# Performance work log

Hardware: AMD Instinct MI355X
Metric: run time of the kernel (lower is better)

The kernel has to match this reference:

```python
import math
import jax, jax.numpy as jnp
import numpy as np

M, D, NL, H, DFF = 14, 128, 2, 4, 512
BS = 256
DK = D // H


def setup_inputs() -> dict:
    key = jax.random.key(0)
    ks = iter(jax.random.split(key, 40))
    def w(shape, s=0.02):
        return jax.random.normal(next(ks), shape, jnp.float32) * s
    return dict(
        src=jax.random.normal(next(ks), (BS, M), jnp.float32),
        t=5,
        fc_w=w((D, 1, 3), 0.3), fc_b=jnp.zeros((D,), jnp.float32),
        gc_w=w((D, 1, 3), 0.3), gc_b=jnp.zeros((D,), jnp.float32),
        ln_w=jnp.ones((D,), jnp.float32), ln_b=jnp.zeros((D,), jnp.float32),
        qw=w((NL, D, D)), qb=jnp.zeros((NL, D), jnp.float32),
        kw=w((NL, D, D)), kb=jnp.zeros((NL, D), jnp.float32),
        vw=w((NL, D, D)), vb=jnp.zeros((NL, D), jnp.float32),
        ow=w((NL, D, D)), ob=jnp.zeros((NL, D), jnp.float32),
        n1a=jnp.ones((NL, D), jnp.float32), n1b=jnp.zeros((NL, D), jnp.float32),
        n2a=jnp.ones((NL, D), jnp.float32), n2b=jnp.zeros((NL, D), jnp.float32),
        w1=w((NL, DFF, D)), b1=jnp.zeros((NL, DFF), jnp.float32),
        w2=w((NL, D, DFF)), b2=jnp.zeros((NL, D), jnp.float32),
        fna=jnp.ones((D,), jnp.float32), fnb=jnp.zeros((D,), jnp.float32),
        out_w=w((1, D)), out_b=jnp.zeros((1,), jnp.float32),
    )


def _conv1d(x, w):  # x [B,1,m], w [O,1,3], padding=1 (SAME)
    return jax.lax.conv_general_dilated(
        x, w, window_strides=(1,), padding=[(1, 1)],
        dimension_numbers=('NCH', 'OIH', 'NCH'))


def _norm(x, a, b, eps=1e-6):
    # torch: alpha*(x-mean)/(std+eps)+bias, std is UNBIASED (ddof=1)
    mu = x.mean(-1, keepdims=True)
    std = jnp.sqrt(jnp.var(x, axis=-1, ddof=1, keepdims=True))
    return a * (x - mu) / (std + eps) + b


def _mha(x, qw, qb, kw, kb, vw, vb, ow, ob):
    bs = x.shape[0]
    def proj(w, b):  # view(bs,-1,h,dk).transpose(1,2) -> [bs,h,s,dk]
        return jnp.swapaxes((x @ w.T + b).reshape(bs, -1, H, DK), 1, 2)
    q, k, v = proj(qw, qb), proj(kw, kb), proj(vw, vb)
    scores = jax.nn.softmax(
        jnp.einsum('bhqd,bhkd->bhqk', q, k) / math.sqrt(DK), axis=-1)
    o = jnp.einsum('bhqk,bhkd->bhqd', scores, v)
    o = jnp.swapaxes(o, 1, 2).reshape(bs, -1, D)
    return o @ ow.T + ob


def _forward(src, fc_w, fc_b, gc_w, gc_b, ln_w, ln_b, qw, qb, kw, kb, vw, vb,
             ow, ob, n1a, n1b, n2a, n2b, w1, b1, w2, b2, fna, fnb,
             out_w, out_b, t):
    # --- GCU embedding: gated conv over the m features, pooled to [bs, D]
    xc = src[:, None, :]                                 # [bs,1,m]
    feat = _conv1d(xc, fc_w) + fc_b[None, :, None]        # [bs,D,m]
    gate = jax.nn.sigmoid(_conv1d(xc, gc_w) + gc_b[None, :, None])
    g = (feat * gate).mean(-1)                            # adaptive_avg_pool1d(.,1)
    mu = g.mean(-1, keepdims=True)                        # torch LayerNorm (biased var)
    var = ((g - mu) ** 2).mean(-1, keepdims=True)
    x = ln_w * (g - mu) / jnp.sqrt(var + 1e-5) + ln_b     # [bs,D]
    # --- positional encoding with scalar position t
    div = jnp.exp(jnp.arange(0, D, 2, dtype=jnp.float32) * (-math.log(10000.0) / D))
    pe = jnp.zeros((D,), jnp.float32).at[0::2].set(jnp.sin(t * div)).at[1::2].set(jnp.cos(t * div))
    x = x * math.sqrt(D) + pe
    # --- encoder layers (layer 0 broadcast-promotes x to [bs,bs,D], faithful to torch)
    for i in range(NL):
        x2 = _norm(x, n1a[i], n1b[i])
        x = x + _mha(x2, qw[i], qb[i], kw[i], kb[i], vw[i], vb[i], ow[i], ob[i])
        x2 = _norm(x, n2a[i], n2b[i])
        x = x + (jax.nn.relu(x2 @ w1[i].T + b1[i]) @ w2[i].T + b2[i])
    x = _norm(x, fna, fnb)
    out = x @ out_w.T + out_b                             # [bs,bs,1]
    return out.squeeze(-1)                                # [bs,bs]


def reference(src, fc_w, fc_b, gc_w, gc_b, ln_w, ln_b, qw, qb, kw, kb, vw, vb,
              ow, ob, n1a, n1b, n2a, n2b, w1, b1, w2, b2, fna, fnb,
              out_w, out_b, t):
    return _forward(src, fc_w, fc_b, gc_w, gc_b, ln_w, ln_b, qw, qb, kw, kb,
                    vw, vb, ow, ob, n1a, n1b, n2a, n2b, w1, b1, w2, b2,
                    fna, fnb, out_w, out_b, t)
```

## Files before the change

kernel.cpp:

```cpp
#include <hip/hip_runtime.h>
#include <math.h>


#define SQRT_D 11.313708498984761f
#define PE_C   0.14391156831212787f
#define INV_SQRT_DK 0.17677669529663687f
#define XF(j,d) (((j) << 7) + ((d) ^ (((j) & 15) << 2)))

typedef _Float16 f16x8 __attribute__((ext_vector_type(8)));
typedef float    f32x4 __attribute__((ext_vector_type(4)));
typedef float    f32x16 __attribute__((ext_vector_type(16)));

#define MFMA16(a, b, c) __builtin_amdgcn_mfma_f32_16x16x32_f16((a), (b), (c), 0, 0, 0)
#define MFMA32(a, b, c) __builtin_amdgcn_mfma_f32_32x32x16_f16((a), (b), (c), 0, 0, 0)

__device__ __forceinline__ unsigned pack2(float a, float b) {
  union { _Float16 h; unsigned short s; } ua, ub;
  ua.h = (_Float16)a; ub.h = (_Float16)b;
  return (unsigned)ua.s | ((unsigned)ub.s << 16);
}

__device__ __forceinline__ f16x8 u4f16x8(unsigned u0, unsigned u1, unsigned u2, unsigned u3) {
  union { unsigned u[4]; f16x8 f; } x;
  x.u[0] = u0; x.u[1] = u1; x.u[2] = u2; x.u[3] = u3;
  return x.f;
}

__device__ __forceinline__ unsigned bperm(int addr, unsigned v) {
  return (unsigned)__builtin_amdgcn_ds_bpermute(addr, (int)v);
}

__device__ __forceinline__ f16x8 make_bfrag(f32x4 cA, f32x4 cB, int aLo, int aHi, int hiSel) {
  unsigned a0 = pack2(cA[0], cA[1]), a1 = pack2(cA[2], cA[3]);
  unsigned b0 = pack2(cB[0], cB[1]), b1 = pack2(cB[2], cB[3]);
  unsigned lA0 = bperm(aLo, a0), lA1 = bperm(aLo, a1);
  unsigned hA0 = bperm(aHi, a0), hA1 = bperm(aHi, a1);
  unsigned lB0 = bperm(aLo, b0), lB1 = bperm(aLo, b1);
  unsigned hB0 = bperm(aHi, b0), hB1 = bperm(aHi, b1);
  return u4f16x8(hiSel ? lB0 : lA0, hiSel ? lB1 : lA1,
                 hiSel ? hB0 : hA0, hiSel ? hB1 : hA1);
}

__device__ __forceinline__ void swapP(unsigned& x, unsigned& y) {
  asm("v_permlane32_swap_b32 %0, %1" : "+v"(x), "+v"(y));
}

__device__ __forceinline__ float crossHalf(float v, int h) {
  unsigned a = __float_as_uint(v), b = a;
  swapP(a, b);
  return __uint_as_float(h ? a : b);
}

__device__ __forceinline__ f16x8 t1frag(const f32x16& c, int kt) {
  const int b = kt * 8;
  unsigned p0 = pack2(c[b + 0], c[b + 1]);
  unsigned p1 = pack2(c[b + 2], c[b + 3]);
  unsigned q0 = pack2(c[b + 4], c[b + 5]);
  unsigned q1 = pack2(c[b + 6], c[b + 7]);
  swapP(p0, q0);
  swapP(p1, q1);
  return u4f16x8(p0, p1, q0, q1);
}

__device__ __forceinline__ f32x16 zero16() {
  f32x16 z;
#pragma unroll
  for (int e = 0; e < 16; ++e) z[e] = 0.f;
  return z;
}

__device__ __forceinline__ f32x16 bias16(const float* __restrict__ b, int base, int h) {
  f32x16 c;
#pragma unroll
  for (int q = 0; q < 4; ++q) {
    f32x4 v = *(const f32x4*)&b[base + q * 8 + 4 * h];
#pragma unroll
    for (int e = 0; e < 4; ++e) c[q * 4 + e] = v[e];
  }
  return c;
}

__device__ __forceinline__ void flush16(float* sX, int row, int D0, int h, const f32x16& c) {
#pragma unroll
  for (int q = 0; q < 4; ++q) {
    float* dst = &sX[XF(row, D0 + q * 8 + 4 * h)];
    f32x4 v = *(const f32x4*)dst;
#pragma unroll
    for (int e = 0; e < 4; ++e) v[e] += c[q * 4 + e];
    *(f32x4*)dst = v;
  }
}

struct P0 { const float *qw, *kw, *vw, *ow, *w1, *w2; _Float16* dst; };

__global__ __launch_bounds__(256) void convblk(P0 p) {
  const int i = blockIdx.x * 256 + threadIdx.x;
  const float* src; int sidx;
  if (i < 262144) {
    const int L = i >> 17;
    const int r = i & 131071;
    if (r < 65536) {
      const int c = r >> 13, rem = r & 8191;
      const int ut = rem >> 12, g = (rem >> 8) & 15, row = (rem >> 3) & 31, e = rem & 7;
      sidx = L * 65536 + (c * 64 + ut * 32 + row) * 128 + g * 8 + e;
      src = p.w1;
    } else {
      const int r2 = r - 65536;
      const int c = r2 >> 13, rem = r2 & 8191;
      const int dt = rem >> 11, g = (rem >> 8) & 7, row = (rem >> 3) & 31, e = rem & 7;
      sidx = L * 65536 + (dt * 32 + row) * 512 + c * 64 + g * 8 + e;
      src = p.w2;
    }
  } else {
    const int j = i - 262144;
    const int m = j >> 14;
    sidx = 16384 + (j & 16383);
    src = (m == 0) ? p.kw : (m == 1 ? p.vw : (m == 2 ? p.qw : p.ow));
  }
  p.dst[i] = (_Float16)src[sidx];
}

struct P1 {
  const float* src; const int* t;
  const float* fc_w; const float* fc_b; const float* gc_w; const float* gc_b;
  const float* ln_w; const float* ln_b;
  const float* n1a; const float* n1b;
  const float* vw; const float* vb; const float* ow; const float* ob;
  float* x0; float* a0;
};

__device__ __forceinline__ float rowReduceSum(float v, volatile float* red, int d) {
#pragma unroll
  for (int off = 32; off > 0; off >>= 1) v += __shfl_xor(v, off, 64);
  if ((d & 63) == 0) red[d >> 6] = v;
  __syncthreads();
  float r = red[0] + red[1];
  __syncthreads();
  return r;
}

__device__ __forceinline__ float dot128s(const float* __restrict__ w,
                                         const float* __restrict__ xs) {
  const float4* __restrict__ w4 = (const float4*)w;
  const float4* __restrict__ x4 = (const float4*)xs;
  float a0 = 0.f, a1 = 0.f, a2 = 0.f, a3 = 0.f;
#pragma unroll
  for (int k = 0; k < 32; k += 4) {
    float4 xv0 = x4[k + 0], xv1 = x4[k + 1], xv2 = x4[k + 2], xv3 = x4[k + 3];
    float4 wv0 = w4[k + 0], wv1 = w4[k + 1], wv2 = w4[k + 2], wv3 = w4[k + 3];
    a0 = fmaf(wv0.w, xv0.w, fmaf(wv0.z, xv0.z, fmaf(wv0.y, xv0.y, fmaf(wv0.x, xv0.x, a0))));
    a1 = fmaf(wv1.w, xv1.w, fmaf(wv1.z, xv1.z, fmaf(wv1.y, xv1.y, fmaf(wv1.x, xv1.x, a1))));
    a2 = fmaf(wv2.w, xv2.w, fmaf(wv2.z, xv2.z, fmaf(wv2.y, xv2.y, fmaf(wv2.x, xv2.x, a2))));
    a3 = fmaf(wv3.w, xv3.w, fmaf(wv3.z, xv3.z, fmaf(wv3.y, xv3.y, fmaf(wv3.x, xv3.x, a3))));
  }
  return (a0 + a1) + (a2 + a3);
}

__global__ __launch_bounds__(256) void prep(P1 p) {
  __shared__ __align__(16) float s_src[2][16];
  __shared__ __align__(16) float s_x2[2][128];
  __shared__ __align__(16) float s_y[2][128];
  __shared__ float s_red[2][2];

  const int tid = threadIdx.x;
  const int rl  = tid >> 7;
  const int d   = tid & 127;
  const int row = blockIdx.x * 2 + rl;
  volatile float* red = s_red[rl];

  if (d < 14) s_src[rl][d + 1] = p.src[row * 14 + d];
  if (d == 14) { s_src[rl][0] = 0.f; s_src[rl][15] = 0.f; }
  __syncthreads();

  const float fw0 = p.fc_w[3*d+0], fw1 = p.fc_w[3*d+1], fw2 = p.fc_w[3*d+2];
  const float gw0 = p.gc_w[3*d+0], gw1 = p.gc_w[3*d+1], gw2 = p.gc_w[3*d+2];
  const float fb = p.fc_b[d], gb = p.gc_b[d];
  float g = 0.f;
#pragma unroll
  for (int m = 0; m < 14; ++m) {
    float xm1 = s_src[rl][m], x0v = s_src[rl][m+1], xp1 = s_src[rl][m+2];
    float f  = fmaf(fw2, xp1, fmaf(fw1, x0v, fmaf(fw0, xm1, fb)));
    float ga = fmaf(gw2, xp1, fmaf(gw1, x0v, fmaf(gw0, xm1, gb)));
    g = fmaf(f, 1.f / (1.f + expf(-ga)), g);
  }
  g *= (1.f / 14.f);

  float mu = rowReduceSum(g, red, d) * (1.f / 128.f);
  float cg = g - mu;
  float var = rowReduceSum(cg * cg, red, d) * (1.f / 128.f);
  float x = fmaf(p.ln_w[d], cg * rsqrtf(var + 1e-5f), p.ln_b[d]);

  const int tval = *p.t;
  {
    int i2 = d >> 1;
    float arg = (float)tval * expf((float)i2 * -PE_C);
    float pe = (d & 1) ? cosf(arg) : sinf(arg);
    x = fmaf(x, SQRT_D, pe);
  }
  p.x0[row * 128 + d] = x;

  float mu1 = rowReduceSum(x, red, d) * (1.f / 128.f);
  float c1 = x - mu1;
  float v1 = rowReduceSum(c1 * c1, red, d) * (1.f / 127.f);
  s_x2[rl][d] = fmaf(p.n1a[d], c1 / (sqrtf(v1) + 1e-6f), p.n1b[d]);
  __syncthreads();

  float y = p.vb[d] + dot128s(p.vw + d * 128, s_x2[rl]);
  s_y[rl][d] = y;
  __syncthreads();
  p.a0[row * 128 + d] = p.ob[d] + dot128s(p.ow + d * 128, s_y[rl]);
}

struct P2 {
  const float* x0; const float* a0;
  const _Float16* wff;
  const _Float16 *wk16, *wv16, *wq16, *wow;
  const float *qb, *kb, *vb, *ob;
  const float *n1a, *n1b, *n2a, *n2b;
  const float *b1, *b2;
  const float *fna, *fnb, *out_w, *out_b;
  float* out;
};

__device__ __forceinline__ void build_x2_pass(const float* sX, int strip, int nt, int l,
    const float* __restrict__ na, const float* __restrict__ nb, f16x8 out[4]) {
  const int l15 = l & 15, q = l >> 4;
  const int row = strip + nt * 16 + l15;
  float sum = 0.f, sq = 0.f;
#pragma unroll
  for (int c4 = 0; c4 < 8; ++c4) {
    f32x4 v = *(const f32x4*)&sX[XF(row, q * 32 + c4 * 4)];
#pragma unroll
    for (int e = 0; e < 4; ++e) { sum += v[e]; sq = fmaf(v[e], v[e], sq); }
  }
  sum += __shfl_xor(sum, 16); sum += __shfl_xor(sum, 32);
  sq  += __shfl_xor(sq, 16);  sq  += __shfl_xor(sq, 32);
  const float mu = sum * (1.f / 128.f);
  const float var = fmaf(-sum, mu, sq) * (1.f / 127.f);
  const float inv = 1.f / (sqrtf(var) + 1e-6f);
#pragma unroll
  for (int kt = 0; kt < 4; ++kt) {
    const int d0 = kt * 32 + q * 8;
    f32x4 xA = *(const f32x4*)&sX[XF(row, d0)];
    f32x4 xB = *(const f32x4*)&sX[XF(row, d0 + 4)];
    f32x4 nA = *(const f32x4*)&na[d0], nB = *(const f32x4*)&na[d0 + 4];
    f32x4 bA = *(const f32x4*)&nb[d0], bB = *(const f32x4*)&nb[d0 + 4];
    float v0 = fmaf(nA[0] * inv, xA[0] - mu, bA[0]);
    float v1 = fmaf(nA[1] * inv, xA[1] - mu, bA[1]);
    float v2 = fmaf(nA[2] * inv, xA[2] - mu, bA[2]);
    float v3 = fmaf(nA[3] * inv, xA[3] - mu, bA[3]);
    float v4 = fmaf(nB[0] * inv, xB[0] - mu, bB[0]);
    float v5 = fmaf(nB[1] * inv, xB[1] - mu, bB[1]);
    float v6 = fmaf(nB[2] * inv, xB[2] - mu, bB[2]);
    float v7 = fmaf(nB[3] * inv, xB[3] - mu, bB[3]);
    out[kt] = u4f16x8(pack2(v0, v1), pack2(v2, v3), pack2(v4, v5), pack2(v6, v7));
  }
}

__device__ __forceinline__ void build_x2(const float* sX, int strip, int l,
    const float* __restrict__ na, const float* __restrict__ nb, f16x8 out[8]) {
  const int h = l >> 5, row = strip + (l & 31);
  f32x4 xs[16];
  float sum = 0.f, sq = 0.f;
#pragma unroll
  for (int s = 0; s < 8; ++s) {
    f32x4 a = *(const f32x4*)&sX[XF(row, s * 16 + 8 * h)];
    f32x4 b = *(const f32x4*)&sX[XF(row, s * 16 + 8 * h + 4)];
    xs[2 * s] = a; xs[2 * s + 1] = b;
#pragma unroll
    for (int e = 0; e < 4; ++e) {
      sum += a[e] + b[e];
      sq = fmaf(a[e], a[e], fmaf(b[e], b[e], sq));
    }
  }
  sum += crossHalf(sum, h);
  sq  += crossHalf(sq, h);
  const float mu = sum * (1.f / 128.f);
  const float var = fmaf(-sum, mu, sq) * (1.f / 127.f);
  const float inv = 1.f / (sqrtf(var) + 1e-6f);
#pragma unroll
  for (int s = 0; s < 8; ++s) {
    const int d0 = s * 16 + 8 * h;
    f32x4 nA = *(const f32x4*)&na[d0], nB = *(const f32x4*)&na[d0 + 4];
    f32x4 bA = *(const f32x4*)&nb[d0], bB = *(const f32x4*)&nb[d0 + 4];
    float v[8];
#pragma unroll
    for (int e = 0; e < 4; ++e) {
      v[e]     = fmaf(nA[e] * inv, xs[2 * s][e] - mu, bA[e]);
      v[4 + e] = fmaf(nB[e] * inv, xs[2 * s + 1][e] - mu, bB[e]);
    }
    out[s] = u4f16x8(pack2(v[0], v[1]), pack2(v[2], v[3]),
                     pack2(v[4], v[5]), pack2(v[6], v[7]));
  }
}

__device__ __forceinline__ void ffn_phase(float* sX, _Float16* aux, int t,
    int strip, int l, const float* __restrict__ na, const float* __restrict__ nb,
    const _Float16* __restrict__ w1blk, const float* __restrict__ b1,
    const _Float16* __restrict__ w2blk, const float* __restrict__ b2) {
  const int h = l >> 5, row = strip + (l & 31);
  f16x8 x2f[8];
  build_x2(sX, strip, l, na, nb, x2f);
#pragma unroll 1
  for (int c = 0; c < 8; ++c) {
    __syncthreads();
    {
      const _Float16* w1c = w1blk + c * 8192;
      const _Float16* w2c = w2blk + c * 8192;
      *(f16x8*)(aux + t * 8)         = *(const f16x8*)(w1c + t * 8);
      *(f16x8*)(aux + 4096 + t * 8)  = *(const f16x8*)(w1c + 4096 + t * 8);
      *(f16x8*)(aux + 8192 + t * 8)  = *(const f16x8*)(w2c + t * 8);
      *(f16x8*)(aux + 12288 + t * 8) = *(const f16x8*)(w2c + 4096 + t * 8);
    }
    __syncthreads();
    f32x16 hacc[2];
#pragma unroll
    for (int ut = 0; ut < 2; ++ut) {
      hacc[ut] = bias16(b1, c * 64 + ut * 32, h);
#pragma unroll
      for (int s = 0; s < 8; ++s) {
        f16x8 a = *(const f16x8*)(aux + ut * 4096 + s * 512 + l * 8);
        hacc[ut] = MFMA32(a, x2f[s], hacc[ut]);
      }
#pragma unroll
      for (int e = 0; e < 16; ++e) hacc[ut][e] = fmaxf(hacc[ut][e], 0.f);
    }
    f16x8 hf[4];
#pragma unroll
    for (int ks = 0; ks < 4; ++ks) hf[ks] = t1frag(hacc[ks >> 1], ks & 1);
#pragma unroll 1
    for (int dt = 0; dt < 4; ++dt) {
      f32x16 oacc = (c == 0) ? bias16(b2, dt * 32, h) : zero16();
#pragma unroll
      for (int ks = 0; ks < 4; ++ks) {
        f16x8 a = *(const f16x8*)(aux + 8192 + dt * 2048 + ks * 512 + l * 8);
        oacc = MFMA32(a, hf[ks], oacc);
      }
      flush16(sX, row, dt * 32, h, oacc);
    }
  }
}

__global__ __launch_bounds__(512) void batchk(P2 p) {
  __shared__ __align__(16) float sX[32768];
  __shared__ __align__(16) _Float16 sAux[16384];

  const int t = threadIdx.x;
  const int i = blockIdx.x;
  const int l = t & 63;
  const int wv = t >> 6;
  const int strip = wv * 32;
  const int l15 = l & 15;
  const int lg = l >> 4;
  const int hiSel = (l >> 5) & 1;
  const int aLo = ((((lg & 1) * 2 + 0) * 16) + l15) * 4;
  const int aHi = ((((lg & 1) * 2 + 1) * 16) + l15) * 4;

  {
    const int j = t >> 1, hf = t & 1;
    const float* xr = p.x0 + j * 128 + hf * 64;
    const float* ar = p.a0 + i * 128 + hf * 64;
#pragma unroll
    for (int c = 0; c < 16; ++c) {
      f32x4 a = *(const f32x4*)(xr + c * 4);
      f32x4 b = *(const f32x4*)(ar + c * 4);
      a += b;
      *(f32x4*)&sX[XF(j, hf * 64 + c * 4)] = a;
    }
  }

  ffn_phase(sX, sAux, t, strip, l, p.n2a, p.n2b, p.wff, p.b1,
            p.wff + 65536, p.b2);

  {
    const float* __restrict__ qb1 = p.qb + 128;
    const float* __restrict__ kb1 = p.kb + 128;
    const float* __restrict__ vb1 = p.vb + 128;
    const float* __restrict__ ob1 = p.ob + 128;

    f16x8 x2f[4][2];
#pragma unroll
    for (int nt = 0; nt < 2; ++nt) {
      f16x8 tmp[4];
      build_x2_pass(sX, strip, nt, l, p.n1a + 128, p.n1b + 128, tmp);
#pragma unroll
      for (int kt = 0; kt < 4; ++kt) x2f[kt][nt] = tmp[kt];
    }

    const int sr = t >> 4, sg = t & 15;

#pragma unroll 1
    for (int h = 0; h < 4; ++h) {
      __syncthreads();
      {
        f16x8 v0 = *(const f16x8*)(p.wk16 + (h * 32 + sr) * 128 + sg * 8);
        *(f16x8*)(sAux + sr * 128 + ((sg ^ (sr & 15)) << 3)) = v0;
        f16x8 v1 = *(const f16x8*)(p.wv16 + (h * 32 + sr) * 128 + sg * 8);
        *(f16x8*)(sAux + 4096 + sr * 128 + ((sg ^ (sr & 15)) << 3)) = v1;
        f16x8 v2 = *(const f16x8*)(p.wq16 + (h * 32 + sr) * 128 + sg * 8);
        *(f16x8*)(sAux + 8192 + sr * 128 + ((sg ^ (sr & 15)) << 3)) = v2;
      }
      __syncthreads();

      f32x4 kacc[2][2], vacc[2][2], qacc[2][2];
#pragma unroll
      for (int mt = 0; mt < 2; ++mt) {
        f32x4 kb4 = *(const f32x4*)&kb1[h * 32 + mt * 16 + lg * 4];
        f32x4 vb4 = *(const f32x4*)&vb1[h * 32 + mt * 16 + lg * 4];
        f32x4 qb4 = *(const f32x4*)&qb1[h * 32 + mt * 16 + lg * 4];
        kacc[mt][0] = kb4; kacc[mt][1] = kb4;
        vacc[mt][0] = vb4; vacc[mt][1] = vb4;
        qacc[mt][0] = qb4; qacc[mt][1] = qb4;
      }
#pragma unroll
      for (int mt = 0; mt < 2; ++mt)
#pragma unroll
        for (int kt = 0; kt < 4; ++kt) {
          const int off = (mt * 16 + l15) * 128 + (((kt * 4 + lg) ^ l15) << 3);
          f16x8 ak = *(const f16x8*)(sAux + off);
          f16x8 av = *(const f16x8*)(sAux + 4096 + off);
          f16x8 aq = *(const f16x8*)(sAux + 8192 + off);
          kacc[mt][0] = MFMA16(ak, x2f[kt][0], kacc[mt][0]);
          kacc[mt][1] = MFMA16(ak, x2f[kt][1], kacc[mt][1]);
          vacc[mt][0] = MFMA16(av, x2f[kt][0], vacc[mt][0]);
          vacc[mt][1] = MFMA16(av, x2f[kt][1], vacc[mt][1]);
          qacc[mt][0] = MFMA16(aq, x2f[kt][0], qacc[mt][0]);
          qacc[mt][1] = MFMA16(aq, x2f[kt][1], qacc[mt][1]);
        }
#pragma unroll
      for (int mt = 0; mt < 2; ++mt)
#pragma unroll
        for (int nt = 0; nt < 2; ++nt)
#pragma unroll
          for (int e = 0; e < 4; ++e) qacc[mt][nt][e] *= INV_SQRT_DK;
      f16x8 qf[2];
      qf[0] = make_bfrag(qacc[0][0], qacc[1][0], aLo, aHi, hiSel);
      qf[1] = make_bfrag(qacc[0][1], qacc[1][1], aLo, aHi, hiSel);
      __syncthreads();

#pragma unroll
      for (int mt = 0; mt < 2; ++mt)
#pragma unroll
        for (int nt = 0; nt < 2; ++nt) {
          const int j = strip + nt * 16 + l15;
          const int db = mt * 16 + lg * 4;
          uint2 w;
          w.x = pack2(kacc[mt][nt][0], kacc[mt][nt][1]);
          w.y = pack2(kacc[mt][nt][2], kacc[mt][nt][3]);
          *(uint2*)(sAux + j * 32 + (db ^ ((j & 3) << 3))) = w;
#pragma unroll
          for (int e = 0; e < 4; ++e) {
            const int d = mt * 16 + lg * 4 + e;
            sAux[8192 + d * 256 + (j ^ ((d & 7) << 3))] = (_Float16)vacc[mt][nt][e];
          }
        }
      __syncthreads();

#pragma unroll
      for (int nt = 0; nt < 2; ++nt) {
        float mrun = -3e38f, lsum = 0.f;
        f32x4 oacc[2];
        { f32x4 z = {0.f, 0.f, 0.f, 0.f}; oacc[0] = z; oacc[1] = z; }
#pragma unroll 1
        for (int ktile = 0; ktile < 8; ++ktile) {
          f32x4 sacc[2];
#pragma unroll
          for (int mt2 = 0; mt2 < 2; ++mt2) {
            const int k = ktile * 32 + mt2 * 16 + l15;
            f16x8 a = *(const f16x8*)(sAux + k * 32 + ((lg * 8) ^ ((k & 3) << 3)));
            f32x4 z = {0.f, 0.f, 0.f, 0.f};
            sacc[mt2] = MFMA16(a, qf[nt], z);
          }
          float tm = -3e38f;
#pragma unroll
          for (int mt2 = 0; mt2 < 2; ++mt2)
#pragma unroll
            for (int e = 0; e < 4; ++e) tm = fmaxf(tm, sacc[mt2][e]);
          tm = fmaxf(tm, __shfl_xor(tm, 16));
          tm = fmaxf(tm, __shfl_xor(tm, 32));
          const float mnew = fmaxf(mrun, tm);
          const float corr = __expf(mrun - mnew);
          float ts = 0.f;
#pragma unroll
          for (int mt2 = 0; mt2 < 2; ++mt2)
#pragma unroll
            for (int e = 0; e < 4; ++e) {
              float ev = __expf(sacc[mt2][e] - mnew);
              sacc[mt2][e] = ev;
              ts += ev;
            }
          ts += __shfl_xor(ts, 16);
          ts += __shfl_xor(ts, 32);
          lsum = fmaf(lsum, corr, ts);
          oacc[0] *= corr; oacc[1] *= corr;
          f16x8 pf = make_bfrag(sacc[0], sacc[1], aLo, aHi, hiSel);
#pragma unroll
          for (int mt2 = 0; mt2 < 2; ++mt2) {
            const int d = mt2 * 16 + l15;
            f16x8 a = *(const f16x8*)(sAux + 8192 + d * 256 + ((ktile * 32 + lg * 8) ^ ((d & 7) << 3)));
            oacc[mt2] = MFMA16(a, pf, oacc[mt2]);
          }
          mrun = mnew;
        }
        const float linv = 1.f / lsum;
        oacc[0] *= linv; oacc[1] *= linv;
        f16x8 of = make_bfrag(oacc[0], oacc[1], aLo, aHi, hiSel);
        f32x4 zacc[8];
#pragma unroll
        for (int mt = 0; mt < 8; ++mt) {
          if (h == 0) zacc[mt] = *(const f32x4*)&ob1[mt * 16 + lg * 4];
          else { f32x4 z = {0.f, 0.f, 0.f, 0.f}; zacc[mt] = z; }
        }
#pragma unroll
        for (int mt = 0; mt < 8; ++mt) {
          f16x8 a = *(const f16x8*)(p.wow + (mt * 16 + l15) * 128 + h * 32 + lg * 8);
          zacc[mt] = MFMA16(a, of, zacc[mt]);
        }
        const int row = strip + nt * 16 + l15;
#pragma unroll
        for (int mt = 0; mt < 8; ++mt) {
          float* dst = &sX[XF(row, mt * 16 + lg * 4)];
          f32x4 v = *(const f32x4*)dst;
          v += zacc[mt];
          *(f32x4*)dst = v;
        }
      }
    }
  }

  ffn_phase(sX, sAux, t, strip, l, p.n2a + 128, p.n2b + 128,
            p.wff + 131072, p.b1 + 512, p.wff + 196608, p.b2 + 128);

  {
    const int r = strip + (l & 31), hf = l >> 5;
    float sum = 0.f, sq = 0.f;
#pragma unroll
    for (int c = 0; c < 16; ++c) {
      f32x4 v = *(const f32x4*)&sX[XF(r, hf * 64 + c * 4)];
#pragma unroll
      for (int e = 0; e < 4; ++e) { sum += v[e]; sq = fmaf(v[e], v[e], sq); }
    }
    sum += __shfl_xor(sum, 32);
    sq  += __shfl_xor(sq, 32);
    float mu = sum * (1.f / 128.f);
    float var = fmaf(-sum, mu, sq) * (1.f / 127.f);
    float inv = 1.f / (sqrtf(var) + 1e-6f);
    float os = 0.f;
#pragma unroll
    for (int c = 0; c < 16; ++c) {
      f32x4 x  = *(const f32x4*)&sX[XF(r, hf * 64 + c * 4)];
      f32x4 fa = *(const f32x4*)&p.fna[hf * 64 + c * 4];
      f32x4 fb = *(const f32x4*)&p.fnb[hf * 64 + c * 4];
      f32x4 wo = *(const f32x4*)&p.out_w[hf * 64 + c * 4];
#pragma unroll
      for (int e = 0; e < 4; ++e)
        os = fmaf(fmaf(fa[e] * inv, x[e] - mu, fb[e]), wo[e], os);
    }
    os += __shfl_xor(os, 32);
    if (l < 32) p.out[i * 256 + r] = os + p.out_b[0];
  }
}

extern "C" void kernel_launch(void* const* d_in, const int* in_sizes, int n_in,
                              void* d_out, int out_size, void* d_ws, size_t ws_size,
                              hipStream_t stream) {
  float* x0 = (float*)d_ws;
  float* a0 = x0 + 32768;
  _Float16* W16 = (_Float16*)((char*)d_ws + 262144);

  P0 p0;
  p0.qw = (const float*)d_in[8];  p0.kw = (const float*)d_in[10];
  p0.vw = (const float*)d_in[12]; p0.ow = (const float*)d_in[14];
  p0.w1 = (const float*)d_in[20]; p0.w2 = (const float*)d_in[22];
  p0.dst = W16;
  convblk<<<dim3(1280), dim3(256), 0, stream>>>(p0);

  P1 p1;
  p1.src  = (const float*)d_in[0];
  p1.t    = (const int*)  d_in[1];
  p1.fc_w = (const float*)d_in[2];  p1.fc_b = (const float*)d_in[3];
  p1.gc_w = (const float*)d_in[4];  p1.gc_b = (const float*)d_in[5];
  p1.ln_w = (const float*)d_in[6];  p1.ln_b = (const float*)d_in[7];
  p1.n1a  = (const float*)d_in[16]; p1.n1b  = (const float*)d_in[17];
  p1.vw   = (const float*)d_in[12]; p1.vb   = (const float*)d_in[13];
  p1.ow   = (const float*)d_in[14]; p1.ob   = (const float*)d_in[15];
  p1.x0 = x0; p1.a0 = a0;
  prep<<<dim3(128), dim3(256), 0, stream>>>(p1);

  P2 p2;
  p2.x0 = x0; p2.a0 = a0;
  p2.wff  = W16;
  p2.wk16 = W16 + 262144;
  p2.wv16 = W16 + 278528;
  p2.wq16 = W16 + 294912;
  p2.wow  = W16 + 311296;
  p2.qb = (const float*)d_in[9];  p2.kb = (const float*)d_in[11];
  p2.vb = (const float*)d_in[13]; p2.ob = (const float*)d_in[15];
  p2.n1a = (const float*)d_in[16]; p2.n1b = (const float*)d_in[17];
  p2.n2a = (const float*)d_in[18]; p2.n2b = (const float*)d_in[19];
  p2.b1 = (const float*)d_in[21];  p2.b2 = (const float*)d_in[23];
  p2.fna = (const float*)d_in[24]; p2.fnb = (const float*)d_in[25];
  p2.out_w = (const float*)d_in[26]; p2.out_b = (const float*)d_in[27];
  p2.out = (float*)d_out;
  batchk<<<dim3(256), dim3(512), 0, stream>>>(p2);
}
```

Measured before the change: 138.5 us.

## Switch layer-1 attention to 32x32 MFMA with fragment-ordered K/V/Q weights

Rewrites the layer-1 attention phase to use 32x32x16 MFMA tiles in place of 16x16x32. K/V/Q weights are pre-permuted into MFMA A-fragment order by the conversion kernel, so each block can copy them linearly into LDS. Fragment transposes now go through t1frag/permlane swaps instead of ds_bpermute. The aim is fewer LDS permute and shuffle operations and fewer MFMA issues per block. In exchange the accumulators grow (f32x16), which raises register pressure, and the LDS swizzle layouts for K and V change.

```diff
diff --git a/kernel.cpp b/kernel.cpp
--- a/kernel.cpp
+++ b/kernel.cpp
@@ -11,7 +11,6 @@
 typedef float    f32x4 __attribute__((ext_vector_type(4)));
 typedef float    f32x16 __attribute__((ext_vector_type(16)));
 
-#define MFMA16(a, b, c) __builtin_amdgcn_mfma_f32_16x16x32_f16((a), (b), (c), 0, 0, 0)
 #define MFMA32(a, b, c) __builtin_amdgcn_mfma_f32_32x32x16_f16((a), (b), (c), 0, 0, 0)
 
 __device__ __forceinline__ unsigned pack2(float a, float b) {
@@ -24,21 +23,6 @@
   union { unsigned u[4]; f16x8 f; } x;
   x.u[0] = u0; x.u[1] = u1; x.u[2] = u2; x.u[3] = u3;
   return x.f;
-}
-
-__device__ __forceinline__ unsigned bperm(int addr, unsigned v) {
-  return (unsigned)__builtin_amdgcn_ds_bpermute(addr, (int)v);
-}
-
-__device__ __forceinline__ f16x8 make_bfrag(f32x4 cA, f32x4 cB, int aLo, int aHi, int hiSel) {
-  unsigned a0 = pack2(cA[0], cA[1]), a1 = pack2(cA[2], cA[3]);
-  unsigned b0 = pack2(cB[0], cB[1]), b1 = pack2(cB[2], cB[3]);
-  unsigned lA0 = bperm(aLo, a0), lA1 = bperm(aLo, a1);
-  unsigned hA0 = bperm(aHi, a0), hA1 = bperm(aHi, a1);
-  unsigned lB0 = bperm(aLo, b0), lB1 = bperm(aLo, b1);
-  unsigned hB0 = bperm(aHi, b0), hB1 = bperm(aHi, b1);
-  return u4f16x8(hiSel ? lB0 : lA0, hiSel ? lB1 : lA1,
-                 hiSel ? hB0 : hA0, hiSel ? hB1 : hA1);
 }
 
 __device__ __forceinline__ void swapP(unsigned& x, unsigned& y) {
@@ -111,11 +95,15 @@
       sidx = L * 65536 + (dt * 32 + row) * 512 + c * 64 + g * 8 + e;
       src = p.w2;
     }
+  } else if (i < 311296) {
+    const int j = i - 262144;
+    const int m = j >> 14, rem = j & 16383;
+    const int hh = rem >> 12, g = (rem >> 8) & 15, row = (rem >> 3) & 31, e = rem & 7;
+    sidx = 16384 + (hh * 32 + row) * 128 + g * 8 + e;
+    src = (m == 0) ? p.kw : (m == 1 ? p.vw : p.qw);
   } else {
-    const int j = i - 262144;
-    const int m = j >> 14;
-    sidx = 16384 + (j & 16383);
-    src = (m == 0) ? p.kw : (m == 1 ? p.vw : (m == 2 ? p.qw : p.ow));
+    sidx = 16384 + (i - 311296);
+    src = p.ow;
   }
   p.dst[i] = (_Float16)src[sidx];
 }
@@ -214,48 +202,14 @@
 struct P2 {
   const float* x0; const float* a0;
   const _Float16* wff;
-  const _Float16 *wk16, *wv16, *wq16, *wow;
+  const _Float16* wkvq;
+  const _Float16* wow;
   const float *qb, *kb, *vb, *ob;
   const float *n1a, *n1b, *n2a, *n2b;
   const float *b1, *b2;
   const float *fna, *fnb, *out_w, *out_b;
   float* out;
 };
-
-__device__ __forceinline__ void build_x2_pass(const float* sX, int strip, int nt, int l,
-    const float* __restrict__ na, const float* __restrict__ nb, f16x8 out[4]) {
-  const int l15 = l & 15, q = l >> 4;
-  const int row = strip + nt * 16 + l15;
-  float sum = 0.f, sq = 0.f;
-#pragma unroll
-  for (int c4 = 0; c4 < 8; ++c4) {
-    f32x4 v = *(const f32x4*)&sX[XF(row, q * 32 + c4 * 4)];
-#pragma unroll
-    for (int e = 0; e < 4; ++e) { sum += v[e]; sq = fmaf(v[e], v[e], sq); }
-  }
-  sum += __shfl_xor(sum, 16); sum += __shfl_xor(sum, 32);
-  sq  += __shfl_xor(sq, 16);  sq  += __shfl_xor(sq, 32);
-  const float mu = sum * (1.f / 128.f);
-  const float var = fmaf(-sum, mu, sq) * (1.f / 127.f);
-  const float inv = 1.f / (sqrtf(var) + 1e-6f);
-#pragma unroll
-  for (int kt = 0; kt < 4; ++kt) {
-    const int d0 = kt * 32 + q * 8;
-    f32x4 xA = *(const f32x4*)&sX[XF(row, d0)];
-    f32x4 xB = *(const f32x4*)&sX[XF(row, d0 + 4)];
-    f32x4 nA = *(const f32x4*)&na[d0], nB = *(const f32x4*)&na[d0 + 4];
-    f32x4 bA = *(const f32x4*)&nb[d0], bB = *(const f32x4*)&nb[d0 + 4];
-    float v0 = fmaf(nA[0] * inv, xA[0] - mu, bA[0]);
-    float v1 = fmaf(nA[1] * inv, xA[1] - mu, bA[1]);
-    float v2 = fmaf(nA[2] * inv, xA[2] - mu, bA[2]);
-    float v3 = fmaf(nA[3] * inv, xA[3] - mu, bA[3]);
-    float v4 = fmaf(nB[0] * inv, xB[0] - mu, bB[0]);
-    float v5 = fmaf(nB[1] * inv, xB[1] - mu, bB[1]);
-    float v6 = fmaf(nB[2] * inv, xB[2] - mu, bB[2]);
-    float v7 = fmaf(nB[3] * inv, xB[3] - mu, bB[3]);
-    out[kt] = u4f16x8(pack2(v0, v1), pack2(v2, v3), pack2(v4, v5), pack2(v6, v7));
-  }
-}
 
 __device__ __forceinline__ void build_x2(const float* sX, int strip, int l,
     const float* __restrict__ na, const float* __restrict__ nb, f16x8 out[8]) {
@@ -350,22 +304,19 @@
   const int l = t & 63;
   const int wv = t >> 6;
   const int strip = wv * 32;
-  const int l15 = l & 15;
-  const int lg = l >> 4;
-  const int hiSel = (l >> 5) & 1;
-  const int aLo = ((((lg & 1) * 2 + 0) * 16) + l15) * 4;
-  const int aHi = ((((lg & 1) * 2 + 1) * 16) + l15) * 4;
+  const int h = l >> 5;
+  const int row = strip + (l & 31);
 
   {
-    const int j = t >> 1, hf = t & 1;
-    const float* xr = p.x0 + j * 128 + hf * 64;
-    const float* ar = p.a0 + i * 128 + hf * 64;
+    const int j = t >> 1, hf2 = t & 1;
+    const float* xr = p.x0 + j * 128 + hf2 * 64;
+    const float* ar = p.a0 + i * 128 + hf2 * 64;
 #pragma unroll
     for (int c = 0; c < 16; ++c) {
       f32x4 a = *(const f32x4*)(xr + c * 4);
       f32x4 b = *(const f32x4*)(ar + c * 4);
       a += b;
-      *(f32x4*)&sX[XF(j, hf * 64 + c * 4)] = a;
+      *(f32x4*)&sX[XF(j, hf2 * 64 + c * 4)] = a;
     }
   }
 
@@ -378,152 +329,93 @@
     const float* __restrict__ vb1 = p.vb + 128;
     const float* __restrict__ ob1 = p.ob + 128;
 
-    f16x8 x2f[4][2];
-#pragma unroll
-    for (int nt = 0; nt < 2; ++nt) {
-      f16x8 tmp[4];
-      build_x2_pass(sX, strip, nt, l, p.n1a + 128, p.n1b + 128, tmp);
-#pragma unroll
-      for (int kt = 0; kt < 4; ++kt) x2f[kt][nt] = tmp[kt];
-    }
-
-    const int sr = t >> 4, sg = t & 15;
+    f16x8 x2f[8];
+    build_x2(sX, strip, l, p.n1a + 128, p.n1b + 128, x2f);
 
 #pragma unroll 1
-    for (int h = 0; h < 4; ++h) {
+    for (int hd = 0; hd < 4; ++hd) {
       __syncthreads();
+#pragma unroll
+      for (int r3 = 0; r3 < 3; ++r3)
+        *(f16x8*)(sAux + r3 * 4096 + t * 8) =
+            *(const f16x8*)(p.wkvq + (r3 * 4 + hd) * 4096 + t * 8);
+      __syncthreads();
+
+      f32x16 kacc = bias16(kb1, hd * 32, h);
+      f32x16 vacc = bias16(vb1, hd * 32, h);
+      f32x16 qacc = bias16(qb1, hd * 32, h);
+#pragma unroll
+      for (int s = 0; s < 8; ++s) {
+        f16x8 ak = *(const f16x8*)(sAux + s * 512 + l * 8);
+        f16x8 av = *(const f16x8*)(sAux + 4096 + s * 512 + l * 8);
+        f16x8 aq = *(const f16x8*)(sAux + 8192 + s * 512 + l * 8);
+        kacc = MFMA32(ak, x2f[s], kacc);
+        vacc = MFMA32(av, x2f[s], vacc);
+        qacc = MFMA32(aq, x2f[s], qacc);
+      }
+#pragma unroll
+      for (int e = 0; e < 16; ++e) qacc[e] *= INV_SQRT_DK;
+      f16x8 qf0 = t1frag(qacc, 0), qf1 = t1frag(qacc, 1);
+      f16x8 kf0 = t1frag(kacc, 0), kf1 = t1frag(kacc, 1);
+      __syncthreads();
+
+      *(f16x8*)(sAux + wv * 1024 + l * 8) = kf0;
+      *(f16x8*)(sAux + wv * 1024 + 512 + l * 8) = kf1;
       {
-        f16x8 v0 = *(const f16x8*)(p.wk16 + (h * 32 + sr) * 128 + sg * 8);
-        *(f16x8*)(sAux + sr * 128 + ((sg ^ (sr & 15)) << 3)) = v0;
-        f16x8 v1 = *(const f16x8*)(p.wv16 + (h * 32 + sr) * 128 + sg * 8);
-        *(f16x8*)(sAux + 4096 + sr * 128 + ((sg ^ (sr & 15)) << 3)) = v1;
-        f16x8 v2 = *(const f16x8*)(p.wq16 + (h * 32 + sr) * 128 + sg * 8);
-        *(f16x8*)(sAux + 8192 + sr * 128 + ((sg ^ (sr & 15)) << 3)) = v2;
+        const int a = (l & 31) >> 3, b = l & 7;
+#pragma unroll
+        for (int reg = 0; reg < 16; ++reg) {
+          const int dv = (reg & 3) + 8 * (reg >> 2) + 4 * h;
+          sAux[8192 + wv * 1024 + a * 256 + ((dv ^ a) << 3) + b] = (_Float16)vacc[reg];
+        }
       }
       __syncthreads();
 
-      f32x4 kacc[2][2], vacc[2][2], qacc[2][2];
-#pragma unroll
-      for (int mt = 0; mt < 2; ++mt) {
-        f32x4 kb4 = *(const f32x4*)&kb1[h * 32 + mt * 16 + lg * 4];
-        f32x4 vb4 = *(const f32x4*)&vb1[h * 32 + mt * 16 + lg * 4];
-        f32x4 qb4 = *(const f32x4*)&qb1[h * 32 + mt * 16 + lg * 4];
-        kacc[mt][0] = kb4; kacc[mt][1] = kb4;
-        vacc[mt][0] = vb4; vacc[mt][1] = vb4;
-        qacc[mt][0] = qb4; qacc[mt][1] = qb4;
-      }
-#pragma unroll
-      for (int mt = 0; mt < 2; ++mt)
-#pragma unroll
-        for (int kt = 0; kt < 4; ++kt) {
-          const int off = (mt * 16 + l15) * 128 + (((kt * 4 + lg) ^ l15) << 3);
-          f16x8 ak = *(const f16x8*)(sAux + off);
-          f16x8 av = *(const f16x8*)(sAux + 4096 + off);
-          f16x8 aq = *(const f16x8*)(sAux + 8192 + off);
-          kacc[mt][0] = MFMA16(ak, x2f[kt][0], kacc[mt][0]);
-          kacc[mt][1] = MFMA16(ak, x2f[kt][1], kacc[mt][1]);
-          vacc[mt][0] = MFMA16(av, x2f[kt][0], vacc[mt][0]);
-          vacc[mt][1] = MFMA16(av, x2f[kt][1], vacc[mt][1]);
-          qacc[mt][0] = MFMA16(aq, x2f[kt][0], qacc[mt][0]);
-          qacc[mt][1] = MFMA16(aq, x2f[kt][1], qacc[mt][1]);
+      float mrun = -3e38f, lsum = 0.f;
+      f32x16 oacc = zero16();
+#pragma unroll 1
+      for (int kt = 0; kt < 8; ++kt) {
+        f32x16 sacc = zero16();
+        sacc = MFMA32(*(const f16x8*)(sAux + kt * 1024 + l * 8), qf0, sacc);
+        sacc = MFMA32(*(const f16x8*)(sAux + kt * 1024 + 512 + l * 8), qf1, sacc);
+        float tm = sacc[0];
+#pragma unroll
+        for (int e = 1; e < 16; ++e) tm = fmaxf(tm, sacc[e]);
+        tm = fmaxf(tm, crossHalf(tm, h));
+        const float mnew = fmaxf(mrun, tm);
+        const float corr = __expf(mrun - mnew);
+        float ts = 0.f;
+#pragma unroll
+        for (int e = 0; e < 16; ++e) {
+          const float ev = __expf(sacc[e] - mnew);
+          sacc[e] = ev;
+          ts += ev;
         }
-#pragma unroll
-      for (int mt = 0; mt < 2; ++mt)
-#pragma unroll
-        for (int nt = 0; nt < 2; ++nt)
-#pragma unroll
-          for (int e = 0; e < 4; ++e) qacc[mt][nt][e] *= INV_SQRT_DK;
-      f16x8 qf[2];
-      qf[0] = make_bfrag(qacc[0][0], qacc[1][0], aLo, aHi, hiSel);
-      qf[1] = make_bfrag(qacc[0][1], qacc[1][1], aLo, aHi, hiSel);
-      __syncthreads();
-
-#pragma unroll
-      for (int mt = 0; mt < 2; ++mt)
-#pragma unroll
-        for (int nt = 0; nt < 2; ++nt) {
-          const int j = strip + nt * 16 + l15;
-          const int db = mt * 16 + lg * 4;
-          uint2 w;
-          w.x = pack2(kacc[mt][nt][0], kacc[mt][nt][1]);
-          w.y = pack2(kacc[mt][nt][2], kacc[mt][nt][3]);
-          *(uint2*)(sAux + j * 32 + (db ^ ((j & 3) << 3))) = w;
-#pragma unroll
-          for (int e = 0; e < 4; ++e) {
-            const int d = mt * 16 + lg * 4 + e;
-            sAux[8192 + d * 256 + (j ^ ((d & 7) << 3))] = (_Float16)vacc[mt][nt][e];
-          }
-        }
-      __syncthreads();
-
-#pragma unroll
-      for (int nt = 0; nt < 2; ++nt) {
-        float mrun = -3e38f, lsum = 0.f;
-        f32x4 oacc[2];
-        { f32x4 z = {0.f, 0.f, 0.f, 0.f}; oacc[0] = z; oacc[1] = z; }
+        ts += crossHalf(ts, h);
+        lsum = fmaf(lsum, corr, ts);
+#pragma unroll
+        for (int e = 0; e < 16; ++e) oacc[e] *= corr;
+        f16x8 pf0 = t1frag(sacc, 0), pf1 = t1frag(sacc, 1);
+        const int ar0 = h, ar1 = 2 + h;
+        f16x8 va0 = *(const f16x8*)(sAux + 8192 + kt * 1024 + ar0 * 256 + (((l & 31) ^ ar0) << 3));
+        f16x8 va1 = *(const f16x8*)(sAux + 8192 + kt * 1024 + ar1 * 256 + (((l & 31) ^ ar1) << 3));
+        oacc = MFMA32(va0, pf0, oacc);
+        oacc = MFMA32(va1, pf1, oacc);
+        mrun = mnew;
+      }
+      const float linv = 1.f / lsum;
+#pragma unroll
+      for (int e = 0; e < 16; ++e) oacc[e] *= linv;
+      f16x8 of0 = t1frag(oacc, 0), of1 = t1frag(oacc, 1);
+
 #pragma unroll 1
-        for (int ktile = 0; ktile < 8; ++ktile) {
-          f32x4 sacc[2];
-#pragma unroll
-          for (int mt2 = 0; mt2 < 2; ++mt2) {
-            const int k = ktile * 32 + mt2 * 16 + l15;
-            f16x8 a = *(const f16x8*)(sAux + k * 32 + ((lg * 8) ^ ((k & 3) << 3)));
-            f32x4 z = {0.f, 0.f, 0.f, 0.f};
-            sacc[mt2] = MFMA16(a, qf[nt], z);
-          }
-          float tm = -3e38f;
-#pragma unroll
-          for (int mt2 = 0; mt2 < 2; ++mt2)
-#pragma unroll
-            for (int e = 0; e < 4; ++e) tm = fmaxf(tm, sacc[mt2][e]);
-          tm = fmaxf(tm, __shfl_xor(tm, 16));
-          tm = fmaxf(tm, __shfl_xor(tm, 32));
-          const float mnew = fmaxf(mrun, tm);
-          const float corr = __expf(mrun - mnew);
-          float ts = 0.f;
-#pragma unroll
-          for (int mt2 = 0; mt2 < 2; ++mt2)
-#pragma unroll
-            for (int e = 0; e < 4; ++e) {
-              float ev = __expf(sacc[mt2][e] - mnew);
-              sacc[mt2][e] = ev;
-              ts += ev;
-            }
-          ts += __shfl_xor(ts, 16);
-          ts += __shfl_xor(ts, 32);
-          lsum = fmaf(lsum, corr, ts);
-          oacc[0] *= corr; oacc[1] *= corr;
-          f16x8 pf = make_bfrag(sacc[0], sacc[1], aLo, aHi, hiSel);
-#pragma unroll
-          for (int mt2 = 0; mt2 < 2; ++mt2) {
-            const int d = mt2 * 16 + l15;
-            f16x8 a = *(const f16x8*)(sAux + 8192 + d * 256 + ((ktile * 32 + lg * 8) ^ ((d & 7) << 3)));
-            oacc[mt2] = MFMA16(a, pf, oacc[mt2]);
-          }
-          mrun = mnew;
-        }
-        const float linv = 1.f / lsum;
-        oacc[0] *= linv; oacc[1] *= linv;
-        f16x8 of = make_bfrag(oacc[0], oacc[1], aLo, aHi, hiSel);
-        f32x4 zacc[8];
-#pragma unroll
-        for (int mt = 0; mt < 8; ++mt) {
-          if (h == 0) zacc[mt] = *(const f32x4*)&ob1[mt * 16 + lg * 4];
-          else { f32x4 z = {0.f, 0.f, 0.f, 0.f}; zacc[mt] = z; }
-        }
-#pragma unroll
-        for (int mt = 0; mt < 8; ++mt) {
-          f16x8 a = *(const f16x8*)(p.wow + (mt * 16 + l15) * 128 + h * 32 + lg * 8);
-          zacc[mt] = MFMA16(a, of, zacc[mt]);
-        }
-        const int row = strip + nt * 16 + l15;
-#pragma unroll
-        for (int mt = 0; mt < 8; ++mt) {
-          float* dst = &sX[XF(row, mt * 16 + lg * 4)];
-          f32x4 v = *(const f32x4*)dst;
-          v += zacc[mt];
-          *(f32x4*)dst = v;
-        }
+      for (int dt = 0; dt < 4; ++dt) {
+        f32x16 zacc = (hd == 0) ? bias16(ob1, dt * 32, h) : zero16();
+        f16x8 a0 = *(const f16x8*)(p.wow + (dt * 32 + (l & 31)) * 128 + hd * 32 + h * 8);
+        f16x8 a1 = *(const f16x8*)(p.wow + (dt * 32 + (l & 31)) * 128 + hd * 32 + 16 + h * 8);
+        zacc = MFMA32(a0, of0, zacc);
+        zacc = MFMA32(a1, of1, zacc);
+        flush16(sX, row, dt * 32, h, zacc);
       }
     }
   }
@@ -590,9 +482,7 @@
   P2 p2;
   p2.x0 = x0; p2.a0 = a0;
   p2.wff  = W16;
-  p2.wk16 = W16 + 262144;
-  p2.wv16 = W16 + 278528;
-  p2.wq16 = W16 + 294912;
+  p2.wkvq = W16 + 262144;
   p2.wow  = W16 + 311296;
   p2.qb = (const float*)d_in[9];  p2.kb = (const float*)d_in[11];
   p2.vb = (const float*)d_in[13]; p2.ob = (const float*)d_in[15];
```

Result: faster. 124.1 us (-10.4%).
